# Optimization experiments

Measured on AMD Instinct MI355X. Metric: run time of the kernel, lower is better.

Reference implementation:

```python
import jax, jax.numpy as jnp
import numpy as np

D_MODEL = 1024
NUM_HEADS = 16


def setup_inputs() -> dict:
    key = jax.random.key(0)
    ks = jax.random.split(key, 5)
    scale = 1.0 / np.sqrt(D_MODEL)
    X = jax.random.normal(ks[0], (4, 2048, D_MODEL), dtype=jnp.float32)
    W_q = jax.random.normal(ks[1], (D_MODEL, D_MODEL), dtype=jnp.float32) * scale
    W_k = jax.random.normal(ks[2], (D_MODEL, D_MODEL), dtype=jnp.float32) * scale
    W_v = jax.random.normal(ks[3], (D_MODEL, D_MODEL), dtype=jnp.float32) * scale
    W_o = jax.random.normal(ks[4], (D_MODEL, D_MODEL), dtype=jnp.float32) * scale
    return {"X": X, "W_q": W_q, "W_k": W_k, "W_v": W_v, "W_o": W_o}


def reference(X, W_q, W_k, W_v, W_o):
    b, s, d_model = X.shape
    h = NUM_HEADS
    d_k = d_model // h
    # Linear projections (y = x @ W^T convention; W stored as [out,in] would be
    # x @ W.T, but with random weights we use x @ W — math is identical in form).
    def split_heads(y):
        return y.reshape(b, s, h, d_k).transpose(0, 2, 1, 3)  # b h s d
    q = split_heads(X @ W_q)
    k = split_heads(X @ W_k)
    v = split_heads(X @ W_v)
    scores = jnp.einsum('bhid,bhjd->bhij', q, k) / jnp.sqrt(jnp.float32(d_k))
    causal = jnp.tril(jnp.ones((s, s), dtype=bool))
    scores = jnp.where(causal[None, None], scores, jnp.float32(-jnp.inf))
    probs = jax.nn.softmax(scores, axis=-1)
    attended = jnp.einsum('bhij,bhjd->bhid', probs, v)
    out = attended.transpose(0, 2, 1, 3).reshape(b, s, d_model)
    return out @ W_o
```

## Files before the change

### kernel.cpp

```cpp
#include <hip/hip_runtime.h>

typedef __bf16 bf16;
typedef __attribute__((ext_vector_type(8))) __bf16 bf16x8;
typedef __attribute__((ext_vector_type(4))) float f32x4;
typedef __attribute__((ext_vector_type(4))) unsigned short u16x4;

#define D_MODEL 1024
#define SEQ     2048
#define NB      4
#define NH      16
#define DK      64
#define MROWS   (NB * SEQ)

#define MFMA_BF16 __builtin_amdgcn_mfma_f32_16x16x32_bf16
#define EXP2F(x) __builtin_amdgcn_exp2f(x)
#define QSCALE 0.18033688011112042f

__device__ __forceinline__ bf16 f2b(float f) {
    union { float f; unsigned u; } c; c.f = f;
    unsigned r = (c.u + 0x7fffu + ((c.u >> 16) & 1u)) >> 16;
    union { unsigned short s; bf16 b; } o; o.s = (unsigned short)r;
    return o.b;
}
__device__ __forceinline__ unsigned short f2u(float f) {
    union { float f; unsigned u; } c; c.f = f;
    return (unsigned short)((c.u + 0x7fffu + ((c.u >> 16) & 1u)) >> 16);
}

__global__ void cvt_f32_bf16_v4(const float* __restrict__ x, bf16* __restrict__ y, int n4) {
    int i = blockIdx.x * blockDim.x + threadIdx.x;
    if (i < n4) {
        float4 v = ((const float4*)x)[i];
        u16x4 o; o[0] = f2u(v.x); o[1] = f2u(v.y); o[2] = f2u(v.z); o[3] = f2u(v.w);
        ((u16x4*)y)[i] = o;
    }
}

__global__ void transpose_w_bf16(const float* __restrict__ w, bf16* __restrict__ wt) {
    __shared__ float tile[32][33];
    const int tx = threadIdx.x & 31, ty = threadIdx.x >> 5;
    const int k0 = blockIdx.y * 32, n0 = blockIdx.x * 32;
#pragma unroll
    for (int i = 0; i < 4; i++)
        tile[ty + i * 8][tx] = w[(size_t)(k0 + ty + i * 8) * 1024 + n0 + tx];
    __syncthreads();
#pragma unroll
    for (int i = 0; i < 4; i++)
        wt[(size_t)(n0 + ty + i * 8) * 1024 + k0 + tx] = f2b(tile[tx][ty + i * 8]);
}

template <int MODE>
__global__ __launch_bounds__(256) void gemm128(const bf16* __restrict__ A,
                                               const bf16* __restrict__ Bt,
                                               void* __restrict__ out) {
    __shared__ __align__(16) bf16 lA[128 * 32];
    __shared__ __align__(16) bf16 lB[128 * 32];

    const int t = threadIdx.x;
    const int wid = t >> 6, lane = t & 63;
    const int ln = lane & 15, qd = lane >> 4;
    const int wm = wid >> 1, wn = wid & 1;
    const int row0 = blockIdx.y * 128, col0 = blockIdx.x * 128;

    const bf16* ga0 = A  + (size_t)(row0 + (t >> 2)) * 1024 + (t & 3) * 8;
    const bf16* ga1 = ga0 + (size_t)64 * 1024;
    const bf16* gb0 = Bt + (size_t)(col0 + (t >> 2)) * 1024 + (t & 3) * 8;
    const bf16* gb1 = gb0 + (size_t)64 * 1024;

    f32x4 acc[4][4];
#pragma unroll
    for (int i = 0; i < 4; i++)
#pragma unroll
        for (int j = 0; j < 4; j++) acc[i][j] = (f32x4){0.f, 0.f, 0.f, 0.f};

    for (int kb = 0; kb < 1024; kb += 32) {
        __builtin_amdgcn_global_load_lds(
            (const __attribute__((address_space(1))) void*)(ga0 + kb),
            (__attribute__((address_space(3))) void*)(&lA[t * 8]), 16, 0, 0);
        __builtin_amdgcn_global_load_lds(
            (const __attribute__((address_space(1))) void*)(ga1 + kb),
            (__attribute__((address_space(3))) void*)(&lA[2048 + t * 8]), 16, 0, 0);
        __builtin_amdgcn_global_load_lds(
            (const __attribute__((address_space(1))) void*)(gb0 + kb),
            (__attribute__((address_space(3))) void*)(&lB[t * 8]), 16, 0, 0);
        __builtin_amdgcn_global_load_lds(
            (const __attribute__((address_space(1))) void*)(gb1 + kb),
            (__attribute__((address_space(3))) void*)(&lB[2048 + t * 8]), 16, 0, 0);
        __syncthreads();

        bf16x8 af[4], bfr[4];
#pragma unroll
        for (int i = 0; i < 4; i++)
            af[i] = *(const bf16x8*)&lA[(wm * 64 + i * 16 + ln) * 32 + qd * 8];
#pragma unroll
        for (int j = 0; j < 4; j++)
            bfr[j] = *(const bf16x8*)&lB[(wn * 64 + j * 16 + ln) * 32 + qd * 8];
#pragma unroll
        for (int i = 0; i < 4; i++)
#pragma unroll
            for (int j = 0; j < 4; j++) {
                if (MODE == 2)
                    acc[i][j] = MFMA_BF16(af[i], bfr[j], acc[i][j], 0, 0, 0);
                else
                    acc[i][j] = MFMA_BF16(bfr[j], af[i], acc[i][j], 0, 0, 0);
            }
        __syncthreads();
    }

#pragma unroll
    for (int i = 0; i < 4; i++)
#pragma unroll
        for (int j = 0; j < 4; j++) {
            if (MODE == 0) {
                int m  = row0 + wm * 64 + i * 16 + ln;
                int n0 = col0 + wn * 64 + j * 16 + qd * 4;
                *(f32x4*)&((float*)out)[(size_t)m * 1024 + n0] = acc[i][j];
            } else if (MODE == 1) {
                int m  = row0 + wm * 64 + i * 16 + ln;
                int n0 = col0 + wn * 64 + j * 16 + qd * 4;
                float scale = (n0 < 1024) ? QSCALE : 1.0f;
                int b = m >> 11, s = m & 2047;
                int h = (n0 & 1023) >> 6, d0 = n0 & 63;
                size_t addr = (((size_t)(b * NH + h) * SEQ + s) * DK + d0)
                              + (size_t)(n0 >> 10) * 8388608;
                u16x4 w;
#pragma unroll
                for (int r = 0; r < 4; r++) w[r] = f2u(acc[i][j][r] * scale);
                *(u16x4*)&((bf16*)out)[addr] = w;
            } else {
                int m0 = row0 + wm * 64 + i * 16 + qd * 4;
                int n  = col0 + wn * 64 + j * 16 + ln;
                int b = m0 >> 11, s0 = m0 & 2047;
                int h = n >> 6, d = n & 63;
                size_t addr = ((size_t)(b * NH + h) * DK + d) * SEQ + s0;
                u16x4 w;
#pragma unroll
                for (int r = 0; r < 4; r++) w[r] = f2u(acc[i][j][r]);
                *(u16x4*)&((bf16*)out)[addr] = w;
            }
        }
}

__global__ __launch_bounds__(256) void attn_kernel(const bf16* __restrict__ Q,
                                                   const bf16* __restrict__ K,
                                                   const bf16* __restrict__ Vt,
                                                   bf16* __restrict__ attn_out) {
    __shared__ __align__(16) bf16 kbuf[2][32 * 64];
    __shared__ __align__(16) bf16 vbuf[2][64 * 32];
    __shared__ __align__(16) bf16 plds[4][16 * 40];

    const int t = threadIdx.x;
    const int wid = t >> 6, lane = t & 63;
    const int ln = lane & 15, qd = lane >> 4;

    const int bid = blockIdx.x;
    const int bh   = ((bid >> 7) << 3) | (bid & 7);
    const int pair = (bid >> 3) & 15;
    const int gA = pair, gB = 31 - pair;
    const int ntA = 2 * gA + 2, ntT = ntA + 2 * gB + 2;

    const bf16* Qh = Q  + (size_t)bh * SEQ * DK;
    const bf16* Kh = K  + (size_t)bh * SEQ * DK;
    const bf16* Vh = Vt + (size_t)bh * DK * SEQ;
    bf16* pw = &plds[wid][0];

    const int kr = t >> 3, kj = t & 7;
    const bf16* kgp = Kh + (size_t)kr * DK + (kj ^ (kr & 7)) * 8;
    const int vr = t >> 2, vj = t & 3;
    const bf16* vgp = Vh + (size_t)vr * SEQ + (vj ^ ((vr >> 1) & 3)) * 8;

    const int swk = ln & 7;
    const int swv = (ln >> 1) & 3;

    f32x4 o[4];
    float l;
    int qw0;
    bf16x8 qf0, qf1;

    auto stage = [&](int kb, int buf) {
        __builtin_amdgcn_global_load_lds(
            (const __attribute__((address_space(1))) void*)(kgp + (size_t)kb * DK),
            (__attribute__((address_space(3))) void*)(&kbuf[buf][t * 8]), 16, 0, 0);
        __builtin_amdgcn_global_load_lds(
            (const __attribute__((address_space(1))) void*)(vgp + kb),
            (__attribute__((address_space(3))) void*)(&vbuf[buf][t * 8]), 16, 0, 0);
    };
    auto initGroup = [&](int g) {
        qw0 = g * 64 + wid * 16;
        qf0 = *(const bf16x8*)(Qh + (size_t)(qw0 + ln) * DK + qd * 8);
        qf1 = *(const bf16x8*)(Qh + (size_t)(qw0 + ln) * DK + 32 + qd * 8);
#pragma unroll
        for (int c = 0; c < 4; c++) o[c] = (f32x4){0.f, 0.f, 0.f, 0.f};
        l = 0.f;
    };
    const int b = bh >> 4, h = bh & 15;
    auto finalize = [&]() {
        float ll = l;
        ll += __shfl_xor(ll, 16);
        ll += __shfl_xor(ll, 32);
        float inv = 1.0f / ll;
        size_t orow = ((size_t)(b * SEQ + qw0 + ln)) * D_MODEL + h * DK;
#pragma unroll
        for (int c = 0; c < 4; c++) {
            u16x4 w;
#pragma unroll
            for (int r = 0; r < 4; r++) w[r] = f2u(o[c][r] * inv);
            *(u16x4*)&attn_out[orow + c * 16 + qd * 4] = w;
        }
    };

    stage(0, 0);
    initGroup(gA);
    int cur = 0;

    for (int i = 0; i < ntT; i++) {
        __syncthreads();
        int nx = i + 1;
        if (nx < ntT) {
            int kbn = (nx < ntA) ? nx * 32 : (nx - ntA) * 32;
            stage(kbn, cur ^ 1);
        }
        const int kb = (i < ntA) ? i * 32 : (i - ntA) * 32;
        const int nkk = min(2, max(0, ((qw0 + 15 - kb) >> 4) + 1));

        if (nkk > 0) {
            bf16x8 vf[4];
#pragma unroll
            for (int c = 0; c < 4; c++)
                vf[c] = *(const bf16x8*)&vbuf[cur][(c * 16 + ln) * 32 + (qd ^ swv) * 8];

            f32x4 st[2];
#pragma unroll
            for (int kk = 0; kk < 2; kk++)
                if (kk < nkk) {
                    const bf16* base = &kbuf[cur][(kk * 16 + ln) * 64];
                    bf16x8 kf0 = *(const bf16x8*)(base + ((qd    ) ^ swk) * 8);
                    bf16x8 kf1 = *(const bf16x8*)(base + ((qd + 4) ^ swk) * 8);
                    f32x4 z = (f32x4){0.f, 0.f, 0.f, 0.f};
                    st[kk] = MFMA_BF16(kf0, qf0, z, 0, 0, 0);
                    st[kk] = MFMA_BF16(kf1, qf1, st[kk], 0, 0, 0);
                }

            float ps = 0.f;
#pragma unroll
            for (int kk = 0; kk < 2; kk++) {
                u16x4 w;
                if (kk < nkk) {
                    f32x4 s = st[kk];
                    if (kb + kk * 16 == qw0) {
#pragma unroll
                        for (int r = 0; r < 4; r++)
                            if (qd * 4 + r > ln) s[r] = -INFINITY;
                    }
                    float p0 = EXP2F(s[0]);
                    float p1 = EXP2F(s[1]);
                    float p2 = EXP2F(s[2]);
                    float p3 = EXP2F(s[3]);
                    ps += (p0 + p1) + (p2 + p3);
                    w[0] = f2u(p0); w[1] = f2u(p1); w[2] = f2u(p2); w[3] = f2u(p3);
                } else {
                    w[0] = 0; w[1] = 0; w[2] = 0; w[3] = 0;
                }
                *(u16x4*)&pw[ln * 40 + kk * 16 + qd * 4] = w;
            }
            l += ps;

            asm volatile("s_waitcnt lgkmcnt(0)" ::: "memory");
            bf16x8 pa = *(const bf16x8*)&pw[ln * 40 + qd * 8];

#pragma unroll
            for (int c = 0; c < 4; c++)
                o[c] = MFMA_BF16(vf[c], pa, o[c], 0, 0, 0);
        }

        if (i == ntA - 1) { finalize(); initGroup(gB); }
        cur ^= 1;
    }
    finalize();
}

extern "C" void kernel_launch(void* const* d_in, const int* in_sizes, int n_in,
                              void* d_out, int out_size, void* d_ws, size_t ws_size,
                              hipStream_t stream) {
    const float* X  = (const float*)d_in[0];
    const float* Wq = (const float*)d_in[1];
    const float* Wk = (const float*)d_in[2];
    const float* Wv = (const float*)d_in[3];
    const float* Wo = (const float*)d_in[4];
    float* out = (float*)d_out;
    char* ws = (char*)d_ws;

    bf16* Xb    = (bf16*)(ws);
    bf16* WqkT  = (bf16*)(ws + (16u << 20));
    bf16* WvT   = (bf16*)(ws + (20u << 20));
    bf16* WoT   = (bf16*)(ws + (22u << 20));
    bf16* Qb    = (bf16*)(ws + (24u << 20));
    bf16* Kb    = (bf16*)(ws + (40u << 20));
    bf16* Vt    = (bf16*)(ws + (56u << 20));
    bf16* Attn  = Xb;

    const int n4 = MROWS * D_MODEL / 4;
    cvt_f32_bf16_v4<<<dim3(n4 / 256), dim3(256), 0, stream>>>(X, Xb, n4);

    dim3 tg(32, 32);
    transpose_w_bf16<<<tg, dim3(256), 0, stream>>>(Wq, WqkT);
    transpose_w_bf16<<<tg, dim3(256), 0, stream>>>(Wk, WqkT + (size_t)1024 * 1024);
    transpose_w_bf16<<<tg, dim3(256), 0, stream>>>(Wv, WvT);
    transpose_w_bf16<<<tg, dim3(256), 0, stream>>>(Wo, WoT);

    gemm128<1><<<dim3(16, 64), dim3(256), 0, stream>>>(Xb, WqkT, Qb);
    gemm128<2><<<dim3(8, 64), dim3(256), 0, stream>>>(Xb, WvT, Vt);

    attn_kernel<<<dim3(1024), dim3(256), 0, stream>>>(Qb, Kb, Vt, Attn);

    gemm128<0><<<dim3(8, 64), dim3(256), 0, stream>>>(Attn, WoT, out);
}
```

Measured before the change: 287.4 us.

## Merge prep kernels, deepen GEMM K-tile to 64 with swizzle, widen attention KV tile

Merges the X conversion and four weight transposes into one prep kernel to cut launch overhead. GEMM staging now loads 64-wide K tiles with an XOR-swizzled LDS layout, halving barriers per K step. The attention kernel now processes 64-key tiles per iteration with swizzled K, V and P buffers, and packs probabilities with a perm instruction. This uses more LDS and wastes more work on the masked diagonal tile, which may reduce occupancy.

```diff
diff --git a/kernel.cpp b/kernel.cpp
--- a/kernel.cpp
+++ b/kernel.cpp
@@ -26,35 +26,49 @@
     union { float f; unsigned u; } c; c.f = f;
     return (unsigned short)((c.u + 0x7fffu + ((c.u >> 16) & 1u)) >> 16);
 }
-
-__global__ void cvt_f32_bf16_v4(const float* __restrict__ x, bf16* __restrict__ y, int n4) {
-    int i = blockIdx.x * blockDim.x + threadIdx.x;
-    if (i < n4) {
-        float4 v = ((const float4*)x)[i];
+__device__ __forceinline__ unsigned fbits(float f) {
+    union { float f; unsigned u; } c; c.f = f; return c.u;
+}
+__device__ __forceinline__ unsigned pack2(float lo, float hi) {
+    return __builtin_amdgcn_perm(fbits(hi), fbits(lo), 0x07060302u);
+}
+
+__global__ void prep_kernel(const float* __restrict__ X,
+                            const float* __restrict__ Wq, const float* __restrict__ Wk,
+                            const float* __restrict__ Wv, const float* __restrict__ Wo,
+                            bf16* __restrict__ Xb, bf16* __restrict__ WqkT,
+                            bf16* __restrict__ WvT, bf16* __restrict__ WoT) {
+    __shared__ float tile[32][33];
+    const int bid = blockIdx.x;
+    if (bid < 8192) {
+        int i = bid * 256 + threadIdx.x;
+        float4 v = ((const float4*)X)[i];
         u16x4 o; o[0] = f2u(v.x); o[1] = f2u(v.y); o[2] = f2u(v.z); o[3] = f2u(v.w);
-        ((u16x4*)y)[i] = o;
+        ((u16x4*)Xb)[i] = o;
+    } else {
+        int r = bid - 8192;
+        int w = r >> 10, tl = r & 1023;
+        const float* src = (w == 0) ? Wq : (w == 1) ? Wk : (w == 2) ? Wv : Wo;
+        bf16* dst = (w == 0) ? WqkT : (w == 1) ? WqkT + (size_t)1024 * 1024
+                  : (w == 2) ? WvT : WoT;
+        const int n0 = (tl & 31) * 32, k0 = (tl >> 5) * 32;
+        const int tx = threadIdx.x & 31, ty = threadIdx.x >> 5;
+#pragma unroll
+        for (int i = 0; i < 4; i++)
+            tile[ty + i * 8][tx] = src[(size_t)(k0 + ty + i * 8) * 1024 + n0 + tx];
+        __syncthreads();
+#pragma unroll
+        for (int i = 0; i < 4; i++)
+            dst[(size_t)(n0 + ty + i * 8) * 1024 + k0 + tx] = f2b(tile[tx][ty + i * 8]);
     }
-}
-
-__global__ void transpose_w_bf16(const float* __restrict__ w, bf16* __restrict__ wt) {
-    __shared__ float tile[32][33];
-    const int tx = threadIdx.x & 31, ty = threadIdx.x >> 5;
-    const int k0 = blockIdx.y * 32, n0 = blockIdx.x * 32;
-#pragma unroll
-    for (int i = 0; i < 4; i++)
-        tile[ty + i * 8][tx] = w[(size_t)(k0 + ty + i * 8) * 1024 + n0 + tx];
-    __syncthreads();
-#pragma unroll
-    for (int i = 0; i < 4; i++)
-        wt[(size_t)(n0 + ty + i * 8) * 1024 + k0 + tx] = f2b(tile[tx][ty + i * 8]);
 }
 
 template <int MODE>
 __global__ __launch_bounds__(256) void gemm128(const bf16* __restrict__ A,
                                                const bf16* __restrict__ Bt,
                                                void* __restrict__ out) {
-    __shared__ __align__(16) bf16 lA[128 * 32];
-    __shared__ __align__(16) bf16 lB[128 * 32];
+    __shared__ __align__(16) bf16 lA[128 * 64];
+    __shared__ __align__(16) bf16 lB[128 * 64];
 
     const int t = threadIdx.x;
     const int wid = t >> 6, lane = t & 63;
@@ -62,10 +76,11 @@
     const int wm = wid >> 1, wn = wid & 1;
     const int row0 = blockIdx.y * 128, col0 = blockIdx.x * 128;
 
-    const bf16* ga0 = A  + (size_t)(row0 + (t >> 2)) * 1024 + (t & 3) * 8;
-    const bf16* ga1 = ga0 + (size_t)64 * 1024;
-    const bf16* gb0 = Bt + (size_t)(col0 + (t >> 2)) * 1024 + (t & 3) * 8;
-    const bf16* gb1 = gb0 + (size_t)64 * 1024;
+    const int srow = t >> 3;
+    const int schunk = (t & 7) ^ (srow & 7);
+    const bf16* ga = A  + (size_t)(row0 + srow) * 1024 + schunk * 8;
+    const bf16* gb = Bt + (size_t)(col0 + srow) * 1024 + schunk * 8;
+    const int swk = ln & 7;
 
     f32x4 acc[4][4];
 #pragma unroll
@@ -73,37 +88,39 @@
 #pragma unroll
         for (int j = 0; j < 4; j++) acc[i][j] = (f32x4){0.f, 0.f, 0.f, 0.f};
 
-    for (int kb = 0; kb < 1024; kb += 32) {
-        __builtin_amdgcn_global_load_lds(
-            (const __attribute__((address_space(1))) void*)(ga0 + kb),
-            (__attribute__((address_space(3))) void*)(&lA[t * 8]), 16, 0, 0);
-        __builtin_amdgcn_global_load_lds(
-            (const __attribute__((address_space(1))) void*)(ga1 + kb),
-            (__attribute__((address_space(3))) void*)(&lA[2048 + t * 8]), 16, 0, 0);
-        __builtin_amdgcn_global_load_lds(
-            (const __attribute__((address_space(1))) void*)(gb0 + kb),
-            (__attribute__((address_space(3))) void*)(&lB[t * 8]), 16, 0, 0);
-        __builtin_amdgcn_global_load_lds(
-            (const __attribute__((address_space(1))) void*)(gb1 + kb),
-            (__attribute__((address_space(3))) void*)(&lB[2048 + t * 8]), 16, 0, 0);
+    for (int kb = 0; kb < 1024; kb += 64) {
+#pragma unroll
+        for (int c = 0; c < 4; c++) {
+            __builtin_amdgcn_global_load_lds(
+                (const __attribute__((address_space(1))) void*)(ga + kb + (size_t)c * 32 * 1024),
+                (__attribute__((address_space(3))) void*)(&lA[t * 8 + c * 2048]), 16, 0, 0);
+            __builtin_amdgcn_global_load_lds(
+                (const __attribute__((address_space(1))) void*)(gb + kb + (size_t)c * 32 * 1024),
+                (__attribute__((address_space(3))) void*)(&lB[t * 8 + c * 2048]), 16, 0, 0);
+        }
         __syncthreads();
 
-        bf16x8 af[4], bfr[4];
-#pragma unroll
-        for (int i = 0; i < 4; i++)
-            af[i] = *(const bf16x8*)&lA[(wm * 64 + i * 16 + ln) * 32 + qd * 8];
-#pragma unroll
-        for (int j = 0; j < 4; j++)
-            bfr[j] = *(const bf16x8*)&lB[(wn * 64 + j * 16 + ln) * 32 + qd * 8];
-#pragma unroll
-        for (int i = 0; i < 4; i++)
-#pragma unroll
-            for (int j = 0; j < 4; j++) {
-                if (MODE == 2)
-                    acc[i][j] = MFMA_BF16(af[i], bfr[j], acc[i][j], 0, 0, 0);
-                else
-                    acc[i][j] = MFMA_BF16(bfr[j], af[i], acc[i][j], 0, 0, 0);
-            }
+#pragma unroll
+        for (int ks = 0; ks < 2; ks++) {
+            bf16x8 af[4], bfr[4];
+#pragma unroll
+            for (int i = 0; i < 4; i++)
+                af[i] = *(const bf16x8*)&lA[(wm * 64 + i * 16 + ln) * 64
+                                            + ((ks * 4 + qd) ^ swk) * 8];
+#pragma unroll
+            for (int j = 0; j < 4; j++)
+                bfr[j] = *(const bf16x8*)&lB[(wn * 64 + j * 16 + ln) * 64
+                                             + ((ks * 4 + qd) ^ swk) * 8];
+#pragma unroll
+            for (int i = 0; i < 4; i++)
+#pragma unroll
+                for (int j = 0; j < 4; j++) {
+                    if (MODE == 2)
+                        acc[i][j] = MFMA_BF16(af[i], bfr[j], acc[i][j], 0, 0, 0);
+                    else
+                        acc[i][j] = MFMA_BF16(bfr[j], af[i], acc[i][j], 0, 0, 0);
+                }
+        }
         __syncthreads();
     }
 
@@ -145,9 +162,9 @@
                                                    const bf16* __restrict__ K,
                                                    const bf16* __restrict__ Vt,
                                                    bf16* __restrict__ attn_out) {
-    __shared__ __align__(16) bf16 kbuf[2][32 * 64];
-    __shared__ __align__(16) bf16 vbuf[2][64 * 32];
-    __shared__ __align__(16) bf16 plds[4][16 * 40];
+    __shared__ __align__(16) bf16 kbuf[2][64 * 64];
+    __shared__ __align__(16) bf16 vbuf[2][64 * 64];
+    __shared__ __align__(16) bf16 plds[4][16 * 64];
 
     const int t = threadIdx.x;
     const int wid = t >> 6, lane = t & 63;
@@ -157,20 +174,18 @@
     const int bh   = ((bid >> 7) << 3) | (bid & 7);
     const int pair = (bid >> 3) & 15;
     const int gA = pair, gB = 31 - pair;
-    const int ntA = 2 * gA + 2, ntT = ntA + 2 * gB + 2;
+    const int ntA = gA + 1, ntT = 33;
 
     const bf16* Qh = Q  + (size_t)bh * SEQ * DK;
     const bf16* Kh = K  + (size_t)bh * SEQ * DK;
     const bf16* Vh = Vt + (size_t)bh * DK * SEQ;
     bf16* pw = &plds[wid][0];
 
-    const int kr = t >> 3, kj = t & 7;
-    const bf16* kgp = Kh + (size_t)kr * DK + (kj ^ (kr & 7)) * 8;
-    const int vr = t >> 2, vj = t & 3;
-    const bf16* vgp = Vh + (size_t)vr * SEQ + (vj ^ ((vr >> 1) & 3)) * 8;
-
+    const int srow = t >> 3;
+    const int schunk = (t & 7) ^ (srow & 7);
+    const bf16* kgp = Kh + (size_t)srow * DK + schunk * 8;
+    const bf16* vgp = Vh + (size_t)srow * SEQ + schunk * 8;
     const int swk = ln & 7;
-    const int swv = (ln >> 1) & 3;
 
     f32x4 o[4];
     float l;
@@ -178,12 +193,15 @@
     bf16x8 qf0, qf1;
 
     auto stage = [&](int kb, int buf) {
-        __builtin_amdgcn_global_load_lds(
-            (const __attribute__((address_space(1))) void*)(kgp + (size_t)kb * DK),
-            (__attribute__((address_space(3))) void*)(&kbuf[buf][t * 8]), 16, 0, 0);
-        __builtin_amdgcn_global_load_lds(
-            (const __attribute__((address_space(1))) void*)(vgp + kb),
-            (__attribute__((address_space(3))) void*)(&vbuf[buf][t * 8]), 16, 0, 0);
+#pragma unroll
+        for (int c = 0; c < 2; c++) {
+            __builtin_amdgcn_global_load_lds(
+                (const __attribute__((address_space(1))) void*)(kgp + (size_t)(kb + c * 32) * DK),
+                (__attribute__((address_space(3))) void*)(&kbuf[buf][t * 8 + c * 2048]), 16, 0, 0);
+            __builtin_amdgcn_global_load_lds(
+                (const __attribute__((address_space(1))) void*)(vgp + (size_t)c * 32 * SEQ + kb),
+                (__attribute__((address_space(3))) void*)(&vbuf[buf][t * 8 + c * 2048]), 16, 0, 0);
+        }
     };
     auto initGroup = [&](int g) {
         qw0 = g * 64 + wid * 16;
@@ -217,21 +235,16 @@
         __syncthreads();
         int nx = i + 1;
         if (nx < ntT) {
-            int kbn = (nx < ntA) ? nx * 32 : (nx - ntA) * 32;
+            int kbn = ((nx < ntA) ? nx : nx - ntA) * 64;
             stage(kbn, cur ^ 1);
         }
-        const int kb = (i < ntA) ? i * 32 : (i - ntA) * 32;
-        const int nkk = min(2, max(0, ((qw0 + 15 - kb) >> 4) + 1));
+        const int kb = ((i < ntA) ? i : i - ntA) * 64;
+        const int nkk = min(4, max(0, ((qw0 + 15 - kb) >> 4) + 1));
 
         if (nkk > 0) {
-            bf16x8 vf[4];
-#pragma unroll
-            for (int c = 0; c < 4; c++)
-                vf[c] = *(const bf16x8*)&vbuf[cur][(c * 16 + ln) * 32 + (qd ^ swv) * 8];
-
-            f32x4 st[2];
-#pragma unroll
-            for (int kk = 0; kk < 2; kk++)
+            f32x4 st[4];
+#pragma unroll
+            for (int kk = 0; kk < 4; kk++)
                 if (kk < nkk) {
                     const bf16* base = &kbuf[cur][(kk * 16 + ln) * 64];
                     bf16x8 kf0 = *(const bf16x8*)(base + ((qd    ) ^ swk) * 8);
@@ -243,8 +256,8 @@
 
             float ps = 0.f;
 #pragma unroll
-            for (int kk = 0; kk < 2; kk++) {
-                u16x4 w;
+            for (int kk = 0; kk < 4; kk++) {
+                unsigned pk0 = 0, pk1 = 0;
                 if (kk < nkk) {
                     f32x4 s = st[kk];
                     if (kb + kk * 16 == qw0) {
@@ -257,20 +270,28 @@
                     float p2 = EXP2F(s[2]);
                     float p3 = EXP2F(s[3]);
                     ps += (p0 + p1) + (p2 + p3);
-                    w[0] = f2u(p0); w[1] = f2u(p1); w[2] = f2u(p2); w[3] = f2u(p3);
-                } else {
-                    w[0] = 0; w[1] = 0; w[2] = 0; w[3] = 0;
+                    pk0 = pack2(p0, p1);
+                    pk1 = pack2(p2, p3);
                 }
-                *(u16x4*)&pw[ln * 40 + kk * 16 + qd * 4] = w;
+                int cw = 2 * kk + (qd >> 1);
+                *(uint2*)&pw[ln * 64 + (cw ^ swk) * 8 + (qd & 1) * 4] =
+                    make_uint2(pk0, pk1);
             }
             l += ps;
 
             asm volatile("s_waitcnt lgkmcnt(0)" ::: "memory");
-            bf16x8 pa = *(const bf16x8*)&pw[ln * 40 + qd * 8];
-
-#pragma unroll
-            for (int c = 0; c < 4; c++)
-                o[c] = MFMA_BF16(vf[c], pa, o[c], 0, 0, 0);
+
+#pragma unroll
+            for (int half = 0; half < 2; half++)
+                if (half == 0 || nkk > 2) {
+                    bf16x8 pa = *(const bf16x8*)&pw[ln * 64 + ((half * 4 + qd) ^ swk) * 8];
+#pragma unroll
+                    for (int c = 0; c < 4; c++) {
+                        bf16x8 vf = *(const bf16x8*)&vbuf[cur][(c * 16 + ln) * 64
+                                        + ((half * 4 + qd) ^ swk) * 8];
+                        o[c] = MFMA_BF16(vf, pa, o[c], 0, 0, 0);
+                    }
+                }
         }
 
         if (i == ntA - 1) { finalize(); initGroup(gB); }
@@ -295,18 +316,12 @@
     bf16* WvT   = (bf16*)(ws + (20u << 20));
     bf16* WoT   = (bf16*)(ws + (22u << 20));
     bf16* Qb    = (bf16*)(ws + (24u << 20));
-    bf16* Kb    = (bf16*)(ws + (40u << 20));
     bf16* Vt    = (bf16*)(ws + (56u << 20));
     bf16* Attn  = Xb;
-
-    const int n4 = MROWS * D_MODEL / 4;
-    cvt_f32_bf16_v4<<<dim3(n4 / 256), dim3(256), 0, stream>>>(X, Xb, n4);
-
-    dim3 tg(32, 32);
-    transpose_w_bf16<<<tg, dim3(256), 0, stream>>>(Wq, WqkT);
-    transpose_w_bf16<<<tg, dim3(256), 0, stream>>>(Wk, WqkT + (size_t)1024 * 1024);
-    transpose_w_bf16<<<tg, dim3(256), 0, stream>>>(Wv, WvT);
-    transpose_w_bf16<<<tg, dim3(256), 0, stream>>>(Wo, WoT);
+    bf16* Kb    = Qb + (size_t)8388608;
+
+    prep_kernel<<<dim3(12288), dim3(256), 0, stream>>>(X, Wq, Wk, Wv, Wo,
+                                                       Xb, WqkT, WvT, WoT);
 
     gemm128<1><<<dim3(16, 64), dim3(256), 0, stream>>>(Xb, WqkT, Qb);
     gemm128<2><<<dim3(8, 64), dim3(256), 0, stream>>>(Xb, WvT, Vt);
```

Measured after the change: 260.8 us. 9.2% less time.
